# Optimization experiments

Measured on AMD Instinct MI355X. Metric: run time of the kernel, lower is better.

Reference implementation:

```python
import jax, jax.numpy as jnp
import numpy as np

T, N, F = 8, 10000, 16
E, H, LD, ENVD = 320000, 64, 3, 5
TEMP, SAL, UI, VI = 11, 12, 13, 14
ENV_IDX = jnp.array([11, 12, 13, 14, 15])
DECAY_KM = 15.0


def _lin(k, o, i, s=0.1):
    return jax.random.normal(k, (o, i), jnp.float32) * s


def setup_inputs() -> dict:
    key = jax.random.key(0)
    ks = jax.random.split(key, 24)
    inp = {
        'node_features_sequence': jax.random.normal(ks[0], (T, N, F), jnp.float32),
        'initial_lice': jax.random.uniform(ks[1], (N, LD), jnp.float32),
        'edge_distance': jax.random.uniform(ks[2], (E,), jnp.float32) * 30.0,
        'edge_direction': jax.random.normal(ks[3], (E, 2), jnp.float32),
        'ee_w1': _lin(ks[4], H, 4), 'ee_b1': jnp.zeros((H,)),
        'ee_w2': _lin(ks[5], H, H), 'ee_b2': jnp.zeros((H,)),
        'at_w1': _lin(ks[6], H, 2 * H), 'at_b1': jnp.zeros((H,)),
        'at_w2': _lin(ks[7], 1, H), 'at_b2': jnp.zeros((1,)),
        'en_w1': _lin(ks[8], H, ENVD), 'en_b1': jnp.zeros((H,)),
        'en_w2': _lin(ks[9], H, H), 'en_b2': jnp.zeros((H,)),
        'fe_w1': _lin(ks[10], 32, 1), 'fe_b1': jnp.zeros((32,)),
        'fe_w2': _lin(ks[11], 32, 32), 'fe_b2': jnp.zeros((32,)),
        'fe_w3': _lin(ks[12], 1, 32), 'fe_b3': jnp.zeros((1,)),
        'gru_wih': _lin(ks[13], 3 * H, H + ENVD + LD),
        'gru_whh': _lin(ks[14], 3 * H, H),
        'gru_bih': jnp.zeros((3 * H,)), 'gru_bhh': jnp.zeros((3 * H,)),
        'de_w1': _lin(ks[15], H, H), 'de_b1': jnp.zeros((H,)),
        'de_w2': _lin(ks[16], LD, H), 'de_b2': jnp.zeros((LD,)),
        'log_beta': jnp.float32(-1.0),
        'temp_sensitivity': jnp.float32(0.1),
        'edge_index': jax.random.randint(ks[17], (2, E), 0, N, jnp.int32),
    }
    return inp


def _mlp2(x, w1, b1, w2, b2):
    return jax.nn.relu(x @ w1.T + b1) @ w2.T + b2


def _gru(x, h, wih, whh, bih, bhh):
    gi = x @ wih.T + bih
    gh = h @ whh.T + bhh
    i_r, i_z, i_n = jnp.split(gi, 3, axis=-1)
    h_r, h_z, h_n = jnp.split(gh, 3, axis=-1)
    r = jax.nn.sigmoid(i_r + h_r)
    z = jax.nn.sigmoid(i_z + h_z)
    n = jnp.tanh(i_n + r * h_n)
    return (1.0 - z) * n + z * h


def reference(node_features_sequence, initial_lice, edge_distance, edge_direction,
              ee_w1, ee_b1, ee_w2, ee_b2, at_w1, at_b1, at_w2, at_b2,
              en_w1, en_b1, en_w2, en_b2, fe_w1, fe_b1, fe_w2, fe_b2, fe_w3, fe_b3,
              gru_wih, gru_whh, gru_bih, gru_bhh, de_w1, de_b1, de_w2, de_b2,
              log_beta, temp_sensitivity, edge_index):
    src, dst = edge_index[0], edge_index[1]
    dist_factor = jnp.exp(-edge_distance / DECAY_KM)
    beta = jnp.exp(log_beta)

    def step(carry, x_t):
        h, lice = carry
        # dynamic edge attributes: [distance, flux+ * decay, temp_src, sal_src]
        u = x_t[src, UI]
        v = x_t[src, VI]
        flux = u * edge_direction[:, 0] + v * edge_direction[:, 1]
        wflux = jnp.clip(flux, 0.0) * dist_factor
        edge_attr = jnp.stack([edge_distance, wflux, x_t[src, TEMP], x_t[src, SAL]], axis=1)
        # edge MLP + attention logits  (E,H)
        ef = _mlp2(edge_attr, ee_w1, ee_b1, ee_w2, ee_b2)
        h_src = h[src]
        logits = _mlp2(jnp.concatenate([ef, h_src], axis=-1), at_w1, at_b1, at_w2, at_b2)[:, 0]
        logits = logits + jnp.log(wflux + 1e-8)
        # per-destination segment softmax
        amax = jax.ops.segment_max(logits, dst, num_segments=N)
        aexp = jnp.exp(logits - amax[dst])
        asum = jax.ops.segment_sum(aexp, dst, num_segments=N)
        aw = aexp / (asum[dst] + 1e-8)
        # flux-weighted lice messages, scatter-add to destinations
        weighted = (aw * lice[src, 0] * beta)[:, None] * h_src  # (E,H)
        pressure = jax.ops.segment_sum(weighted, dst, num_segments=N)  # (N,H)
        # environment + fecundity
        env = x_t[:, ENV_IDX]
        temp_norm = (x_t[:, TEMP] - 10.0) / 5.0
        fec = jax.nn.softplus(
            _mlp2(jax.nn.relu(temp_norm[:, None] @ fe_w1.T + fe_b1), fe_w2, fe_b2, fe_w3, fe_b3))[:, 0]
        env_enc = _mlp2(env, en_w1, en_b1, en_w2, en_b2)
        din = jnp.concatenate([env_enc + pressure, env, lice], axis=-1)
        h_new = _gru(din, h, gru_wih, gru_whh, gru_bih, gru_bhh)
        lice_base = jax.nn.softplus(_mlp2(h_new, de_w1, de_b1, de_w2, de_b2))
        lice_new = lice_base * (1.0 + temp_sensitivity * (fec[:, None] - 1.0))
        return (h_new, lice_new), lice_new

    h0 = jnp.zeros((N, H), jnp.float32)
    _, traj = jax.lax.scan(step, (h0, initial_lice), node_features_sequence)
    return traj  # (T, N, feature_dim)
```

## Files before the change

### kernel.cpp

```cpp
#include <hip/hip_runtime.h>
#include <math.h>

#define T_STEPS 8
#define NNODES 10000
#define NFEAT 16
#define NEDGES 320000
#define HDIM 64
#define LDIM 3
#define CAP 128

typedef _Float16 f16x8 __attribute__((ext_vector_type(8)));
typedef _Float16 f16x4 __attribute__((ext_vector_type(4)));
typedef float f32x4 __attribute__((ext_vector_type(4)));

__device__ __forceinline__ float sigmoidf_(float x){ return 1.f/(1.f+__expf(-x)); }
__device__ __forceinline__ float softplusf_(float x){ return fmaxf(x,0.f)+log1pf(__expf(-fabsf(x))); }
__device__ __forceinline__ float tanhf_(float x){ return 2.f*sigmoidf_(2.f*x)-1.f; }


__global__ void __launch_bounds__(256) k_prep(
    const float* __restrict__ ee_w2, const float* __restrict__ ee_b2,
    const float* __restrict__ at_w1, const float* __restrict__ at_b1,
    _Float16* __restrict__ P_Mhi, _Float16* __restrict__ P_Mlo,
    float* __restrict__ cvec)
{
    int i = blockIdx.x*256 + threadIdx.x;
    if (i >= 64*64) return;
    int m = i>>6, j = i&63;
    float acc = 0.f;
    #pragma unroll 8
    for (int k=0;k<64;++k) acc += ee_w2[k*64+m]*at_w1[j*128+k];
    int ks = m>>5;
    int lane = ((m>>3)&3)*16 + (j&15);
    int elem = m&7;
    int fi = (j>>4)*2 + ks;
    _Float16 hi = (_Float16)acc;
    P_Mhi[(fi*64+lane)*8+elem] = hi;
    P_Mlo[(fi*64+lane)*8+elem] = (_Float16)(acc - (float)hi);
    if (m == 0){
        float c = at_b1[j];
        #pragma unroll 8
        for (int k=0;k<64;++k) c += ee_b2[k]*at_w1[j*128+k];
        cvec[j] = c;
    }
}

__device__ __forceinline__ void packB(const float* __restrict__ W, int ldw, int koff, int K, int NKS,
                                      _Float16* __restrict__ Dhi, _Float16* __restrict__ Dlo, int li){
    int elem = li & 7;
    int lane = (li >> 3) & 63;
    int fi   = li >> 9;
    int jt = fi / NKS, ks = fi % NKS;
    int j = jt*16 + (lane & 15);
    int k = ks*32 + ((lane>>4)&3)*8 + elem;
    float v = (k < K) ? W[j*ldw + koff + k] : 0.f;
    _Float16 hi = (_Float16)v;
    Dhi[li] = hi;
    Dlo[li] = (_Float16)(v - (float)hi);
}

__global__ void __launch_bounds__(256) k_init(
    const float* __restrict__ init_lice, const float* __restrict__ cvec,
    const float* __restrict__ en_w1, const float* __restrict__ en_w2,
    const float* __restrict__ gru_wih, const float* __restrict__ gru_whh,
    const float* __restrict__ de_w1, const float* __restrict__ at_w1,
    float* __restrict__ h, float* __restrict__ lice, float* __restrict__ G,
    _Float16* __restrict__ F_en1h, _Float16* __restrict__ F_en1l,
    _Float16* __restrict__ F_enh,  _Float16* __restrict__ F_enl,
    _Float16* __restrict__ F_ihh,  _Float16* __restrict__ F_ihl,
    _Float16* __restrict__ F_hhh,  _Float16* __restrict__ F_hhl,
    _Float16* __restrict__ F_deh,  _Float16* __restrict__ F_del,
    _Float16* __restrict__ F_a2h,  _Float16* __restrict__ F_a2l,
    int* __restrict__ counts)
{
    int i = blockIdx.x*256 + threadIdx.x;
    if (i < NNODES*HDIM){ h[i] = 0.f; G[i] = cvec[i&63]; }
    if (i < NNODES*LDIM) lice[i] = init_lice[i];
    if (i < NNODES) counts[i] = 0;
    if (i < 2048)       packB(en_w1,   5,  0,  5, 1, F_en1h, F_en1l, i);
    else if (i < 6144)  packB(en_w2,  64,  0, 64, 2, F_enh,  F_enl,  i-2048);
    else if (i < 24576) packB(gru_wih,72,  0, 72, 3, F_ihh,  F_ihl,  i-6144);
    else if (i < 36864) packB(gru_whh,64,  0, 64, 2, F_hhh,  F_hhl,  i-24576);
    else if (i < 40960) packB(de_w1,  64,  0, 64, 2, F_deh,  F_del,  i-36864);
    else if (i < 45056) packB(at_w1, 128, 64, 64, 2, F_a2h,  F_a2l,  i-40960);
}

__global__ void __launch_bounds__(256) k_fec(
    const float* __restrict__ nfs,
    const float* __restrict__ fe_w1, const float* __restrict__ fe_b1,
    const float* __restrict__ fe_w2, const float* __restrict__ fe_b2,
    const float* __restrict__ fe_w3, const float* __restrict__ fe_b3,
    float* __restrict__ fec_arr)
{
    int i = blockIdx.x*256 + threadIdx.x;
    if (i >= T_STEPS*NNODES) return;
    float temp = nfs[(size_t)i*NFEAT + 11];
    float tn = (temp - 10.f)*(1.f/5.f);
    float a[32];
    #pragma unroll
    for (int k=0;k<32;++k) a[k] = fmaxf(tn*fe_w1[k] + fe_b1[k], 0.f);
    float o = fe_b3[0];
    #pragma unroll 4
    for (int l=0;l<32;++l){
        float b = fe_b2[l];
        #pragma unroll
        for (int k=0;k<32;++k) b += a[k]*fe_w2[l*32+k];
        o += fmaxf(b, 0.f)*fe_w3[l];
    }
    fec_arr[i] = softplusf_(o);
}

__global__ void __launch_bounds__(256) k_hist(const int* __restrict__ ei_dst, int* __restrict__ counts){
    int e = blockIdx.x*256 + threadIdx.x;
    if (e < NEDGES) atomicAdd(&counts[ei_dst[e]], 1);
}

__global__ void __launch_bounds__(1024) k_scan(const int* __restrict__ counts,
                                               int* __restrict__ rowptr, int* __restrict__ cursor){
    __shared__ int sums[1024];
    int t = threadIdx.x;
    const int CH = 10;
    int c0 = t*CH;
    int s = 0;
    if (c0 < NNODES){
        #pragma unroll
        for (int i=0;i<CH;i++) s += counts[c0+i];
    }
    sums[t] = s;
    __syncthreads();
    for (int off=1; off<1024; off<<=1){
        int v = (t>=off) ? sums[t-off] : 0;
        __syncthreads();
        sums[t] += v;
        __syncthreads();
    }
    if (c0 < NNODES){
        int run = (t==0) ? 0 : sums[t-1];
        for (int i=0;i<CH;i++){ rowptr[c0+i] = run; run += counts[c0+i]; cursor[c0+i] = 0; }
        if (t == (NNODES/CH)-1) rowptr[NNODES] = run;
    }
}

__global__ void __launch_bounds__(256) k_scatter(const int* __restrict__ ei_dst,
        const int* __restrict__ rowptr, int* __restrict__ cursor, int* __restrict__ perm){
    int e = blockIdx.x*256 + threadIdx.x;
    if (e >= NEDGES) return;
    int d = ei_dst[e];
    int pos = rowptr[d] + atomicAdd(&cursor[d], 1);
    perm[pos] = e;
}

__global__ void __launch_bounds__(256) k_permg(
    const int* __restrict__ perm, const int* __restrict__ ei_src,
    const float* __restrict__ dist, const float* __restrict__ dirn,
    int* __restrict__ src_perm, float* __restrict__ dist_p, float* __restrict__ dirn_p)
{
    int i = blockIdx.x*256 + threadIdx.x;
    if (i >= NEDGES) return;
    int e = perm[i];
    src_perm[i] = ei_src[e];
    dist_p[i] = dist[e];
    float2 dd = *reinterpret_cast<const float2*>(dirn + 2*e);
    *reinterpret_cast<float2*>(dirn_p + 2*i) = dd;
}


__global__ void __launch_bounds__(256,2) k_edge_mfma(
    const float* __restrict__ xt, const float* __restrict__ G,
    const int* __restrict__ src_perm,
    const float* __restrict__ dist_p, const float* __restrict__ dirn_p,
    const float* __restrict__ ee_w1, const float* __restrict__ ee_b1,
    const _Float16* __restrict__ P_Mhi, const _Float16* __restrict__ P_Mlo,
    const float* __restrict__ at_w2, const float* __restrict__ at_b2,
    float* __restrict__ logits)
{
    __shared__ __align__(16) _Float16 smh[36864];
    float* smf = (float*)smh;

    const int tid = threadIdx.x;
    const int wv = tid>>6, lane = tid&63;
    const int e = blockIdx.x*256 + tid;

    f16x8 bh[4][2], bl[4][2];
    #pragma unroll
    for (int jt=0;jt<4;++jt){
        #pragma unroll
        for (int ks=0;ks<2;++ks){
            bh[jt][ks] = *(const f16x8*)(P_Mhi + (((jt*2+ks)*64 + lane)*8));
            bl[jt][ks] = *(const f16x8*)(P_Mlo + (((jt*2+ks)*64 + lane)*8));
        }
    }

    const int src = src_perm[e];
    const float d  = dist_p[e];
    float2 dir2 = *reinterpret_cast<const float2*>(dirn_p + 2*e);
    float temp = xt[src*NFEAT+11];
    float4 q  = *reinterpret_cast<const float4*>(xt + src*NFEAT + 12);
    float flux = q.y*dir2.x + q.z*dir2.y;
    float wflux = fmaxf(flux, 0.f) * __expf(-d*(1.f/15.f));
    const float a0 = d, a1 = wflux, a2 = temp, a3 = q.x;
    const float lbias = at_b2[0] + __logf(wflux + 1e-8f);

    #pragma unroll
    for (int kb=0;kb<8;++kb){
        f16x8 hv, lv;
        #pragma unroll
        for (int i=0;i<8;++i){
            const int m = kb*8+i;
            float4 w1 = *reinterpret_cast<const float4*>(ee_w1 + m*4);
            float r = fmaxf(ee_b1[m] + a0*w1.x + a1*w1.y + a2*w1.z + a3*w1.w, 0.f);
            _Float16 hi = (_Float16)r;
            hv[i] = hi;
            lv[i] = (_Float16)(r - (float)hi);
        }
        *(f16x8*)(smh + tid*72 + kb*8)         = hv;
        *(f16x8*)(smh + 18432 + tid*72 + kb*8) = lv;
    }
    asm volatile("s_waitcnt lgkmcnt(0)" ::: "memory");

    f32x4 c[4][4];
    #pragma unroll
    for (int et=0;et<4;++et)
        #pragma unroll
        for (int jt=0;jt<4;++jt)
            c[et][jt] = (f32x4){0.f,0.f,0.f,0.f};

    #pragma unroll
    for (int et=0;et<4;++et){
        #pragma unroll
        for (int ks=0;ks<2;++ks){
            const int row = wv*64 + et*16 + (lane&15);
            f16x8 ah = *(const f16x8*)(smh + row*72 + ks*32 + (lane>>4)*8);
            f16x8 al = *(const f16x8*)(smh + 18432 + row*72 + ks*32 + (lane>>4)*8);
            #pragma unroll
            for (int jt=0;jt<4;++jt){
                c[et][jt] = __builtin_amdgcn_mfma_f32_16x16x32_f16(ah, bh[jt][ks], c[et][jt], 0,0,0);
                c[et][jt] = __builtin_amdgcn_mfma_f32_16x16x32_f16(ah, bl[jt][ks], c[et][jt], 0,0,0);
                c[et][jt] = __builtin_amdgcn_mfma_f32_16x16x32_f16(al, bh[jt][ks], c[et][jt], 0,0,0);
            }
        }
    }
    asm volatile("s_waitcnt lgkmcnt(0)" ::: "memory");

    #pragma unroll
    for (int et=0;et<4;++et){
        #pragma unroll
        for (int jt=0;jt<4;++jt){
            #pragma unroll
            for (int i=0;i<4;++i){
                const int rl = et*16 + ((lane>>4)&3)*4 + i;
                const int col = jt*16 + (lane&15);
                const int idx = (et < 2) ? (wv*2304 + rl*68 + col)
                                         : (9216 + wv*2304 + (rl-32)*68 + col);
                smf[idx] = c[et][jt][i];
            }
        }
    }
    asm volatile("s_waitcnt lgkmcnt(0)" ::: "memory");

    const int el = tid & 63;
    const float* crow = smf + ((el < 32) ? (wv*2304 + el*68)
                                         : (9216 + wv*2304 + (el-32)*68));
    const float4* G4 = reinterpret_cast<const float4*>(G + src*HDIM);
    float logit = lbias;
    #pragma unroll
    for (int jj=0;jj<16;++jj){
        float4 cv = *reinterpret_cast<const float4*>(crow + jj*4);
        float4 gv = G4[jj];
        float4 w4 = *reinterpret_cast<const float4*>(at_w2 + jj*4);
        logit += w4.x*fmaxf(cv.x+gv.x,0.f) + w4.y*fmaxf(cv.y+gv.y,0.f)
               + w4.z*fmaxf(cv.z+gv.z,0.f) + w4.w*fmaxf(cv.w+gv.w,0.f);
    }
    logits[e] = logit;
}


__global__ void __launch_bounds__(256) k_softmax_pressure(
    const float* __restrict__ logits, const float* __restrict__ h,
    const float* __restrict__ lice, const int* __restrict__ src_perm,
    const int* __restrict__ rowptr,
    const float* __restrict__ log_beta,
    float* __restrict__ pressure)
{
    __shared__ float swgt[CAP];
    __shared__ int   ssrc[CAP];
    __shared__ float sred[4][64];
    __shared__ float sredm[4], sreds[4];

    const int node = blockIdx.x;
    const int tid = threadIdx.x;
    const int wid = tid >> 6;
    const int lane = tid & 63;
    const int start = rowptr[node], end = rowptr[node+1];
    const int deg = end - start;
    const int nfast = deg < CAP ? deg : CAP;

    float m = -INFINITY;
    for (int i=start+tid; i<end; i+=256){
        float lg = logits[i];
        int o = i - start;
        if (o < CAP){ swgt[o] = lg; ssrc[o] = src_perm[i]; }
        m = fmaxf(m, lg);
    }
    #pragma unroll
    for (int off=32; off>=1; off>>=1) m = fmaxf(m, __shfl_xor(m, off));
    if (lane == 0) sredm[wid] = m;
    __syncthreads();
    m = fmaxf(fmaxf(sredm[0], sredm[1]), fmaxf(sredm[2], sredm[3]));

    float s = 0.f;
    for (int i=start+tid; i<end; i+=256){
        int o = i - start;
        float lg = (o < CAP) ? swgt[o] : logits[i];
        s += __expf(lg - m);
    }
    #pragma unroll
    for (int off=32; off>=1; off>>=1) s += __shfl_xor(s, off);
    if (lane == 0) sreds[wid] = s;
    __syncthreads();
    s = (sreds[0]+sreds[1])+(sreds[2]+sreds[3]);

    const float binv = __expf(log_beta[0])/(s + 1e-8f);

    for (int o=tid; o<nfast; o+=256){
        int sc = ssrc[o];
        swgt[o] = __expf(swgt[o] - m) * binv * lice[sc*LDIM];
    }
    __syncthreads();

    float p = 0.f;
    for (int o=wid; o<nfast; o+=4)
        p += swgt[o]*h[ssrc[o]*HDIM + lane];
    for (int i=start+CAP+wid; i<end; i+=4){
        int sc = src_perm[i];
        float wg = __expf(logits[i]-m)*binv*lice[sc*LDIM];
        p += wg*h[sc*HDIM+lane];
    }
    sred[wid][lane] = p;
    __syncthreads();
    if (wid == 0)
        pressure[node*HDIM + lane] = (sred[0][lane]+sred[1][lane])+(sred[2][lane]+sred[3][lane]);
}


__global__ void __launch_bounds__(256,1) k_node_mfma(
    const float* __restrict__ xt,
    float* __restrict__ h, float* __restrict__ lice,
    const float* __restrict__ pressure,
    const _Float16* __restrict__ F_en1h, const _Float16* __restrict__ F_en1l,
    const _Float16* __restrict__ F_enh,  const _Float16* __restrict__ F_enl,
    const _Float16* __restrict__ F_ihh,  const _Float16* __restrict__ F_ihl,
    const _Float16* __restrict__ F_hhh,  const _Float16* __restrict__ F_hhl,
    const _Float16* __restrict__ F_deh,  const _Float16* __restrict__ F_del,
    const _Float16* __restrict__ F_a2h,  const _Float16* __restrict__ F_a2l,
    const float* __restrict__ en_b1, const float* __restrict__ en_b2,
    const float* __restrict__ gru_bih, const float* __restrict__ gru_bhh,
    const float* __restrict__ de_b1, const float* __restrict__ de_w2, const float* __restrict__ de_b2,
    const float* __restrict__ cvec, const float* __restrict__ fec_t,
    const float* __restrict__ temp_sens,
    float* __restrict__ G, float* __restrict__ out_t)
{
    __shared__ __align__(16) _Float16 Ah_hi[64*72], Ah_lo[64*72];
    __shared__ __align__(16) _Float16 At_hi[64*72], At_lo[64*72];
    __shared__ __align__(16) _Float16 Ad_hi[64*104], Ad_lo[64*104];
    __shared__ float s_pd[64*64];
    __shared__ float s_fec[64];

    const int tid = threadIdx.x;
    const int w = tid>>6, lane = tid&63;
    const int l15 = lane & 15, lq = (lane>>4)&3;
    const int n0 = blockIdx.x*64;
    const int nvalid = (NNODES - n0 < 64) ? (NNODES - n0) : 64;

    #pragma unroll
    for (int it=0; it<4; ++it){
        int idx = tid + it*256;
        int node = idx>>4, k4 = idx&15;
        int nc = n0 + (node < nvalid ? node : nvalid-1);
        float4 hv = *reinterpret_cast<const float4*>(h + nc*64 + k4*4);
        float4 pv = *reinterpret_cast<const float4*>(pressure + nc*64 + k4*4);
        *reinterpret_cast<float4*>(s_pd + node*64 + k4*4) = pv;
        f16x4 hh, hl;
        hh[0]=(_Float16)hv.x; hh[1]=(_Float16)hv.y; hh[2]=(_Float16)hv.z; hh[3]=(_Float16)hv.w;
        hl[0]=(_Float16)(hv.x-(float)hh[0]); hl[1]=(_Float16)(hv.y-(float)hh[1]);
        hl[2]=(_Float16)(hv.z-(float)hh[2]); hl[3]=(_Float16)(hv.w-(float)hh[3]);
        *reinterpret_cast<f16x4*>(Ah_hi + node*72 + k4*4) = hh;
        *reinterpret_cast<f16x4*>(Ah_lo + node*72 + k4*4) = hl;
    }
    if (w == 0){
        int nc = n0 + (lane < nvalid ? lane : nvalid-1);
        float ev[8];
        ev[0]=xt[nc*16+11]; ev[1]=xt[nc*16+12]; ev[2]=xt[nc*16+13];
        ev[3]=xt[nc*16+14]; ev[4]=xt[nc*16+15];
        ev[5]=lice[nc*3+0]; ev[6]=lice[nc*3+1]; ev[7]=lice[nc*3+2];
        s_fec[lane] = fec_t[nc];
        f16x8 eh, el;
        #pragma unroll
        for (int i=0;i<8;++i){ eh[i]=(_Float16)ev[i]; el[i]=(_Float16)(ev[i]-(float)eh[i]); }
        *reinterpret_cast<f16x8*>(Ad_hi + lane*104 + 64) = eh;
        *reinterpret_cast<f16x8*>(Ad_lo + lane*104 + 64) = el;
        f16x8 zz = {(_Float16)0,(_Float16)0,(_Float16)0,(_Float16)0,
                    (_Float16)0,(_Float16)0,(_Float16)0,(_Float16)0};
        *reinterpret_cast<f16x8*>(Ad_hi + lane*104 + 72) = zz;
        *reinterpret_cast<f16x8*>(Ad_hi + lane*104 + 80) = zz;
        *reinterpret_cast<f16x8*>(Ad_hi + lane*104 + 88) = zz;
        *reinterpret_cast<f16x8*>(Ad_lo + lane*104 + 72) = zz;
        *reinterpret_cast<f16x8*>(Ad_lo + lane*104 + 80) = zz;
        *reinterpret_cast<f16x8*>(Ad_lo + lane*104 + 88) = zz;
    }
    __syncthreads();

    {
        f16x8 bh = *(const f16x8*)(F_en1h + (w*64+lane)*8);
        f16x8 bl = *(const f16x8*)(F_en1l + (w*64+lane)*8);
        f32x4 c[4];
        #pragma unroll
        for (int et=0;et<4;++et) c[et] = (f32x4){0.f,0.f,0.f,0.f};
        #pragma unroll
        for (int et=0;et<4;++et){
            int row = et*16 + l15;
            f16x8 ah = *(const f16x8*)(Ad_hi + row*104 + 64 + lq*8);
            f16x8 al = *(const f16x8*)(Ad_lo + row*104 + 64 + lq*8);
            c[et] = __builtin_amdgcn_mfma_f32_16x16x32_f16(ah, bh, c[et],0,0,0);
            c[et] = __builtin_amdgcn_mfma_f32_16x16x32_f16(ah, bl, c[et],0,0,0);
            c[et] = __builtin_amdgcn_mfma_f32_16x16x32_f16(al, bh, c[et],0,0,0);
        }
        int col = w*16 + l15;
        float b1 = en_b1[col];
        #pragma unroll
        for (int et=0;et<4;++et){
            #pragma unroll
            for (int i=0;i<4;++i){
                int row = et*16 + lq*4 + i;
                float v = fmaxf(c[et][i] + b1, 0.f);
                _Float16 hi = (_Float16)v;
                At_hi[row*72+col] = hi;
                At_lo[row*72+col] = (_Float16)(v-(float)hi);
            }
        }
    }
    __syncthreads();

    {
        f32x4 c[4];
        #pragma unroll
        for (int et=0;et<4;++et) c[et] = (f32x4){0.f,0.f,0.f,0.f};
        #pragma unroll
        for (int ks=0; ks<2; ++ks){
            f16x8 bh = *(const f16x8*)(F_enh + ((w*2+ks)*64+lane)*8);
            f16x8 bl = *(const f16x8*)(F_enl + ((w*2+ks)*64+lane)*8);
            #pragma unroll
            for (int et=0;et<4;++et){
                int row = et*16 + l15;
                f16x8 ah = *(const f16x8*)(At_hi + row*72 + ks*32 + lq*8);
                f16x8 al = *(const f16x8*)(At_lo + row*72 + ks*32 + lq*8);
                c[et] = __builtin_amdgcn_mfma_f32_16x16x32_f16(ah, bh, c[et],0,0,0);
                c[et] = __builtin_amdgcn_mfma_f32_16x16x32_f16(ah, bl, c[et],0,0,0);
                c[et] = __builtin_amdgcn_mfma_f32_16x16x32_f16(al, bh, c[et],0,0,0);
            }
        }
        int col = w*16 + l15;
        float b2 = en_b2[col];
        #pragma unroll
        for (int et=0;et<4;++et){
            #pragma unroll
            for (int i=0;i<4;++i){
                int row = et*16 + lq*4 + i;
                float v = c[et][i] + b2 + s_pd[row*64+col];
                _Float16 hi = (_Float16)v;
                Ad_hi[row*104+col] = hi;
                Ad_lo[row*104+col] = (_Float16)(v-(float)hi);
            }
        }
    }
    __syncthreads();

    f32x4 Cr[4], Cz[4], Ci[4], Chn[4];
    {
        int col = w*16 + l15;
        float br = gru_bih[col]     + gru_bhh[col];
        float bz = gru_bih[64+col]  + gru_bhh[64+col];
        float bi = gru_bih[128+col];
        float bn = gru_bhh[128+col];
        #pragma unroll
        for (int et=0;et<4;++et){
            Cr[et]  = (f32x4){br,br,br,br};
            Cz[et]  = (f32x4){bz,bz,bz,bz};
            Ci[et]  = (f32x4){bi,bi,bi,bi};
            Chn[et] = (f32x4){bn,bn,bn,bn};
        }
    }
    #pragma unroll
    for (int ks=0; ks<3; ++ks){
        f16x8 ah[4], al[4];
        #pragma unroll
        for (int et=0;et<4;++et){
            int row = et*16 + l15;
            ah[et] = *(const f16x8*)(Ad_hi + row*104 + ks*32 + lq*8);
            al[et] = *(const f16x8*)(Ad_lo + row*104 + ks*32 + lq*8);
        }
        {
            int fi = w*3 + ks;
            f16x8 bh = *(const f16x8*)(F_ihh + (fi*64+lane)*8);
            f16x8 bl = *(const f16x8*)(F_ihl + (fi*64+lane)*8);
            #pragma unroll
            for (int et=0;et<4;++et){
                Cr[et] = __builtin_amdgcn_mfma_f32_16x16x32_f16(ah[et], bh, Cr[et],0,0,0);
                Cr[et] = __builtin_amdgcn_mfma_f32_16x16x32_f16(ah[et], bl, Cr[et],0,0,0);
                Cr[et] = __builtin_amdgcn_mfma_f32_16x16x32_f16(al[et], bh, Cr[et],0,0,0);
            }
        }
        {
            int fi = (4+w)*3 + ks;
            f16x8 bh = *(const f16x8*)(F_ihh + (fi*64+lane)*8);
            f16x8 bl = *(const f16x8*)(F_ihl + (fi*64+lane)*8);
            #pragma unroll
            for (int et=0;et<4;++et){
                Cz[et] = __builtin_amdgcn_mfma_f32_16x16x32_f16(ah[et], bh, Cz[et],0,0,0);
                Cz[et] = __builtin_amdgcn_mfma_f32_16x16x32_f16(ah[et], bl, Cz[et],0,0,0);
                Cz[et] = __builtin_amdgcn_mfma_f32_16x16x32_f16(al[et], bh, Cz[et],0,0,0);
            }
        }
        {
            int fi = (8+w)*3 + ks;
            f16x8 bh = *(const f16x8*)(F_ihh + (fi*64+lane)*8);
            f16x8 bl = *(const f16x8*)(F_ihl + (fi*64+lane)*8);
            #pragma unroll
            for (int et=0;et<4;++et){
                Ci[et] = __builtin_amdgcn_mfma_f32_16x16x32_f16(ah[et], bh, Ci[et],0,0,0);
                Ci[et] = __builtin_amdgcn_mfma_f32_16x16x32_f16(ah[et], bl, Ci[et],0,0,0);
                Ci[et] = __builtin_amdgcn_mfma_f32_16x16x32_f16(al[et], bh, Ci[et],0,0,0);
            }
        }
    }
    #pragma unroll
    for (int ks=0; ks<2; ++ks){
        f16x8 ah[4], al[4];
        #pragma unroll
        for (int et=0;et<4;++et){
            int row = et*16 + l15;
            ah[et] = *(const f16x8*)(Ah_hi + row*72 + ks*32 + lq*8);
            al[et] = *(const f16x8*)(Ah_lo + row*72 + ks*32 + lq*8);
        }
        {
            int fi = w*2 + ks;
            f16x8 bh = *(const f16x8*)(F_hhh + (fi*64+lane)*8);
            f16x8 bl = *(const f16x8*)(F_hhl + (fi*64+lane)*8);
            #pragma unroll
            for (int et=0;et<4;++et){
                Cr[et] = __builtin_amdgcn_mfma_f32_16x16x32_f16(ah[et], bh, Cr[et],0,0,0);
                Cr[et] = __builtin_amdgcn_mfma_f32_16x16x32_f16(ah[et], bl, Cr[et],0,0,0);
                Cr[et] = __builtin_amdgcn_mfma_f32_16x16x32_f16(al[et], bh, Cr[et],0,0,0);
            }
        }
        {
            int fi = (4+w)*2 + ks;
            f16x8 bh = *(const f16x8*)(F_hhh + (fi*64+lane)*8);
            f16x8 bl = *(const f16x8*)(F_hhl + (fi*64+lane)*8);
            #pragma unroll
            for (int et=0;et<4;++et){
                Cz[et] = __builtin_amdgcn_mfma_f32_16x16x32_f16(ah[et], bh, Cz[et],0,0,0);
                Cz[et] = __builtin_amdgcn_mfma_f32_16x16x32_f16(ah[et], bl, Cz[et],0,0,0);
                Cz[et] = __builtin_amdgcn_mfma_f32_16x16x32_f16(al[et], bh, Cz[et],0,0,0);
            }
        }
        {
            int fi = (8+w)*2 + ks;
            f16x8 bh = *(const f16x8*)(F_hhh + (fi*64+lane)*8);
            f16x8 bl = *(const f16x8*)(F_hhl + (fi*64+lane)*8);
            #pragma unroll
            for (int et=0;et<4;++et){
                Chn[et] = __builtin_amdgcn_mfma_f32_16x16x32_f16(ah[et], bh, Chn[et],0,0,0);
                Chn[et] = __builtin_amdgcn_mfma_f32_16x16x32_f16(ah[et], bl, Chn[et],0,0,0);
                Chn[et] = __builtin_amdgcn_mfma_f32_16x16x32_f16(al[et], bh, Chn[et],0,0,0);
            }
        }
    }

    float hnv[16];
    {
        const int coln = w*16 + l15;
        #pragma unroll
        for (int et=0;et<4;++et){
            #pragma unroll
            for (int i=0;i<4;++i){
                int row = et*16 + lq*4 + i;
                float r  = sigmoidf_(Cr[et][i]);
                float z  = sigmoidf_(Cz[et][i]);
                float nn = tanhf_(Ci[et][i] + r*Chn[et][i]);
                float hold = (float)Ah_hi[row*72+coln] + (float)Ah_lo[row*72+coln];
                hnv[et*4+i] = (1.f-z)*nn + z*hold;
            }
        }
    }
    __syncthreads();
    {
        const int coln = w*16 + l15;
        #pragma unroll
        for (int et=0;et<4;++et){
            #pragma unroll
            for (int i=0;i<4;++i){
                int row = et*16 + lq*4 + i;
                float v = hnv[et*4+i];
                if (row < nvalid) h[(n0+row)*HDIM + coln] = v;
                _Float16 hi = (_Float16)v;
                Ah_hi[row*72+coln] = hi;
                Ah_lo[row*72+coln] = (_Float16)(v-(float)hi);
            }
        }
    }
    __syncthreads();

    {
        int col = w*16 + l15;
        float bd = de_b1[col], bg = cvec[col];
        f32x4 Cd[4], Cg[4];
        #pragma unroll
        for (int et=0;et<4;++et){ Cd[et]=(f32x4){bd,bd,bd,bd}; Cg[et]=(f32x4){bg,bg,bg,bg}; }
        #pragma unroll
        for (int ks=0;ks<2;++ks){
            f16x8 ah[4], al[4];
            #pragma unroll
            for (int et=0;et<4;++et){
                int row = et*16 + l15;
                ah[et] = *(const f16x8*)(Ah_hi + row*72 + ks*32 + lq*8);
                al[et] = *(const f16x8*)(Ah_lo + row*72 + ks*32 + lq*8);
            }
            f16x8 dh = *(const f16x8*)(F_deh + ((w*2+ks)*64+lane)*8);
            f16x8 dl = *(const f16x8*)(F_del + ((w*2+ks)*64+lane)*8);
            f16x8 gh = *(const f16x8*)(F_a2h + ((w*2+ks)*64+lane)*8);
            f16x8 gl = *(const f16x8*)(F_a2l + ((w*2+ks)*64+lane)*8);
            #pragma unroll
            for (int et=0;et<4;++et){
                Cd[et] = __builtin_amdgcn_mfma_f32_16x16x32_f16(ah[et], dh, Cd[et],0,0,0);
                Cd[et] = __builtin_amdgcn_mfma_f32_16x16x32_f16(ah[et], dl, Cd[et],0,0,0);
                Cd[et] = __builtin_amdgcn_mfma_f32_16x16x32_f16(al[et], dh, Cd[et],0,0,0);
                Cg[et] = __builtin_amdgcn_mfma_f32_16x16x32_f16(ah[et], gh, Cg[et],0,0,0);
                Cg[et] = __builtin_amdgcn_mfma_f32_16x16x32_f16(ah[et], gl, Cg[et],0,0,0);
                Cg[et] = __builtin_amdgcn_mfma_f32_16x16x32_f16(al[et], gh, Cg[et],0,0,0);
            }
        }
        #pragma unroll
        for (int et=0;et<4;++et){
            #pragma unroll
            for (int i=0;i<4;++i){
                int row = et*16 + lq*4 + i;
                if (row < nvalid) G[(n0+row)*HDIM + col] = Cg[et][i];
                s_pd[row*64+col] = fmaxf(Cd[et][i], 0.f);
            }
        }
    }
    __syncthreads();

    {
        float ts = temp_sens[0];
        #pragma unroll 1
        for (int m=0;m<16;++m){
            int node = w*16 + m;
            float d1v = s_pd[node*64 + lane];
            float s0 = d1v*de_w2[lane];
            float s1 = d1v*de_w2[64+lane];
            float s2 = d1v*de_w2[128+lane];
            #pragma unroll
            for (int off=32; off>=1; off>>=1){
                s0 += __shfl_xor(s0,off);
                s1 += __shfl_xor(s1,off);
                s2 += __shfl_xor(s2,off);
            }
            if (lane < LDIM && node < nvalid){
                float fec = s_fec[node];
                float oi = (lane==0?s0:(lane==1?s1:s2)) + de_b2[lane];
                float lb = softplusf_(oi);
                float ln = lb*(1.f + ts*(fec-1.f));
                lice[(n0+node)*LDIM+lane] = ln;
                out_t[(n0+node)*LDIM+lane] = ln;
            }
        }
    }
}


extern "C" void kernel_launch(void* const* d_in, const int* in_sizes, int n_in,
                              void* d_out, int out_size, void* d_ws, size_t ws_size,
                              hipStream_t stream) {
    const float* nfs       = (const float*)d_in[0];
    const float* init_lice = (const float*)d_in[1];
    const float* dist      = (const float*)d_in[2];
    const float* dirn      = (const float*)d_in[3];
    const float* ee_w1     = (const float*)d_in[4];
    const float* ee_b1     = (const float*)d_in[5];
    const float* ee_w2     = (const float*)d_in[6];
    const float* ee_b2     = (const float*)d_in[7];
    const float* at_w1     = (const float*)d_in[8];
    const float* at_b1     = (const float*)d_in[9];
    const float* at_w2     = (const float*)d_in[10];
    const float* at_b2     = (const float*)d_in[11];
    const float* en_w1     = (const float*)d_in[12];
    const float* en_b1     = (const float*)d_in[13];
    const float* en_w2     = (const float*)d_in[14];
    const float* en_b2     = (const float*)d_in[15];
    const float* fe_w1     = (const float*)d_in[16];
    const float* fe_b1     = (const float*)d_in[17];
    const float* fe_w2     = (const float*)d_in[18];
    const float* fe_b2     = (const float*)d_in[19];
    const float* fe_w3     = (const float*)d_in[20];
    const float* fe_b3     = (const float*)d_in[21];
    const float* gru_wih   = (const float*)d_in[22];
    const float* gru_whh   = (const float*)d_in[23];
    const float* gru_bih   = (const float*)d_in[24];
    const float* gru_bhh   = (const float*)d_in[25];
    const float* de_w1     = (const float*)d_in[26];
    const float* de_b1     = (const float*)d_in[27];
    const float* de_w2     = (const float*)d_in[28];
    const float* de_b2     = (const float*)d_in[29];
    const float* log_beta  = (const float*)d_in[30];
    const float* temp_sens = (const float*)d_in[31];
    const int*   ei        = (const int*)d_in[32];
    const int*   ei_src = ei;
    const int*   ei_dst = ei + NEDGES;
    float* out = (float*)d_out;

    float* wsf = (float*)d_ws;
    size_t off = 0;
    float* h        = wsf + off; off += (size_t)NNODES*HDIM;
    float* lice     = wsf + off; off += (size_t)NNODES*LDIM + 2;
    off = (off + 3) & ~(size_t)3;
    float* logits   = wsf + off; off += (size_t)NEDGES;
    float* pressure = wsf + off; off += (size_t)NNODES*HDIM;
    float* G        = wsf + off; off += (size_t)NNODES*HDIM;
    float* cvec     = wsf + off; off += 64;
    _Float16* P_Mhi = (_Float16*)(wsf + off); off += 2048;
    _Float16* P_Mlo = (_Float16*)(wsf + off); off += 2048;
    _Float16* F_en1h= (_Float16*)(wsf + off); off += 1024;
    _Float16* F_en1l= (_Float16*)(wsf + off); off += 1024;
    _Float16* F_enh = (_Float16*)(wsf + off); off += 2048;
    _Float16* F_enl = (_Float16*)(wsf + off); off += 2048;
    _Float16* F_ihh = (_Float16*)(wsf + off); off += 9216;
    _Float16* F_ihl = (_Float16*)(wsf + off); off += 9216;
    _Float16* F_hhh = (_Float16*)(wsf + off); off += 6144;
    _Float16* F_hhl = (_Float16*)(wsf + off); off += 6144;
    _Float16* F_deh = (_Float16*)(wsf + off); off += 2048;
    _Float16* F_del = (_Float16*)(wsf + off); off += 2048;
    _Float16* F_a2h = (_Float16*)(wsf + off); off += 2048;
    _Float16* F_a2l = (_Float16*)(wsf + off); off += 2048;
    float* fec_arr  = wsf + off; off += (size_t)T_STEPS*NNODES;
    float* dist_p   = wsf + off; off += NEDGES;
    float* dirn_p   = wsf + off; off += 2*NEDGES;
    int* src_perm = (int*)(wsf + off); off += NEDGES;
    int* counts = (int*)(wsf + off); off += NNODES;
    int* rowptr = (int*)(wsf + off); off += NNODES+1;
    int* cursor = (int*)(wsf + off); off += NNODES;
    int* perm   = (int*)(wsf + off); off += NEDGES;

    k_prep<<<16,256,0,stream>>>(ee_w2, ee_b2, at_w1, at_b1, P_Mhi, P_Mlo, cvec);
    k_init<<<2500,256,0,stream>>>(init_lice, cvec,
                                  en_w1, en_w2, gru_wih, gru_whh, de_w1, at_w1,
                                  h, lice, G,
                                  F_en1h, F_en1l, F_enh, F_enl,
                                  F_ihh, F_ihl, F_hhh, F_hhl,
                                  F_deh, F_del, F_a2h, F_a2l,
                                  counts);
    k_fec<<<(T_STEPS*NNODES+255)/256,256,0,stream>>>(nfs, fe_w1, fe_b1, fe_w2, fe_b2,
                                                     fe_w3, fe_b3, fec_arr);
    k_hist<<<1250,256,0,stream>>>(ei_dst, counts);
    k_scan<<<1,1024,0,stream>>>(counts, rowptr, cursor);
    k_scatter<<<1250,256,0,stream>>>(ei_dst, rowptr, cursor, perm);
    k_permg<<<1250,256,0,stream>>>(perm, ei_src, dist, dirn, src_perm, dist_p, dirn_p);

    const int node_blocks = (NNODES + 63)/64;
    for (int t=0; t<T_STEPS; ++t){
        const float* xt = nfs + (size_t)t*NNODES*NFEAT;
        k_edge_mfma<<<1250,256,0,stream>>>(xt, G, src_perm, dist_p, dirn_p,
                                           ee_w1, ee_b1, P_Mhi, P_Mlo,
                                           at_w2, at_b2, logits);
        k_softmax_pressure<<<NNODES,256,0,stream>>>(logits, h, lice, src_perm,
                                                    rowptr, log_beta, pressure);
        k_node_mfma<<<node_blocks,256,0,stream>>>(xt, h, lice, pressure,
                                           F_en1h, F_en1l, F_enh, F_enl,
                                           F_ihh, F_ihl, F_hhh, F_hhl,
                                           F_deh, F_del, F_a2h, F_a2l,
                                           en_b1, en_b2, gru_bih, gru_bhh,
                                           de_b1, de_w2, de_b2,
                                           cvec, fec_arr + (size_t)t*NNODES,
                                           temp_sens,
                                           G, out + (size_t)t*NNODES*LDIM);
    }
}
```

Baseline: 835.0 us.

## Shrink node-update kernel tile to 16 nodes per block for more blocks

The node MLP/GRU kernel now handles 16 nodes per 256-thread block instead of 64, so each wave does one MFMA row tile instead of four. This gives 625 blocks instead of 157, which spreads the work across more CUs and cuts register and LDS use (launch bounds raised to 4 blocks per CU). The cost is that each block reloads the same weight fragments for fewer nodes, and the bounds checks are dropped on the assumption that N divides evenly by 16.

```diff
diff --git a/kernel.cpp b/kernel.cpp
--- a/kernel.cpp
+++ b/kernel.cpp
@@ -343,7 +343,7 @@
 }
 
 
-__global__ void __launch_bounds__(256,1) k_node_mfma(
+__global__ void __launch_bounds__(256,4) k_node_mfma(
     const float* __restrict__ xt,
     float* __restrict__ h, float* __restrict__ lice,
     const float* __restrict__ pressure,
@@ -360,23 +360,20 @@
     const float* __restrict__ temp_sens,
     float* __restrict__ G, float* __restrict__ out_t)
 {
-    __shared__ __align__(16) _Float16 Ah_hi[64*72], Ah_lo[64*72];
-    __shared__ __align__(16) _Float16 At_hi[64*72], At_lo[64*72];
-    __shared__ __align__(16) _Float16 Ad_hi[64*104], Ad_lo[64*104];
-    __shared__ float s_pd[64*64];
-    __shared__ float s_fec[64];
+    __shared__ __align__(16) _Float16 Ah_hi[16*72], Ah_lo[16*72];
+    __shared__ __align__(16) _Float16 At_hi[16*72], At_lo[16*72];
+    __shared__ __align__(16) _Float16 Ad_hi[16*104], Ad_lo[16*104];
+    __shared__ float s_pd[16*64];
+    __shared__ float s_fec[16];
 
     const int tid = threadIdx.x;
     const int w = tid>>6, lane = tid&63;
     const int l15 = lane & 15, lq = (lane>>4)&3;
-    const int n0 = blockIdx.x*64;
-    const int nvalid = (NNODES - n0 < 64) ? (NNODES - n0) : 64;
-
-    #pragma unroll
-    for (int it=0; it<4; ++it){
-        int idx = tid + it*256;
-        int node = idx>>4, k4 = idx&15;
-        int nc = n0 + (node < nvalid ? node : nvalid-1);
+    const int n0 = blockIdx.x*16;
+
+    {
+        int node = tid>>4, k4 = tid&15;
+        int nc = n0 + node;
         float4 hv = *reinterpret_cast<const float4*>(h + nc*64 + k4*4);
         float4 pv = *reinterpret_cast<const float4*>(pressure + nc*64 + k4*4);
         *reinterpret_cast<float4*>(s_pd + node*64 + k4*4) = pv;
@@ -387,8 +384,8 @@
         *reinterpret_cast<f16x4*>(Ah_hi + node*72 + k4*4) = hh;
         *reinterpret_cast<f16x4*>(Ah_lo + node*72 + k4*4) = hl;
     }
-    if (w == 0){
-        int nc = n0 + (lane < nvalid ? lane : nvalid-1);
+    if (w == 0 && lane < 16){
+        int nc = n0 + lane;
         float ev[8];
         ev[0]=xt[nc*16+11]; ev[1]=xt[nc*16+12]; ev[2]=xt[nc*16+13];
         ev[3]=xt[nc*16+14]; ev[4]=xt[nc*16+15];
@@ -413,200 +410,145 @@
     {
         f16x8 bh = *(const f16x8*)(F_en1h + (w*64+lane)*8);
         f16x8 bl = *(const f16x8*)(F_en1l + (w*64+lane)*8);
-        f32x4 c[4];
-        #pragma unroll
-        for (int et=0;et<4;++et) c[et] = (f32x4){0.f,0.f,0.f,0.f};
-        #pragma unroll
-        for (int et=0;et<4;++et){
-            int row = et*16 + l15;
-            f16x8 ah = *(const f16x8*)(Ad_hi + row*104 + 64 + lq*8);
-            f16x8 al = *(const f16x8*)(Ad_lo + row*104 + 64 + lq*8);
-            c[et] = __builtin_amdgcn_mfma_f32_16x16x32_f16(ah, bh, c[et],0,0,0);
-            c[et] = __builtin_amdgcn_mfma_f32_16x16x32_f16(ah, bl, c[et],0,0,0);
-            c[et] = __builtin_amdgcn_mfma_f32_16x16x32_f16(al, bh, c[et],0,0,0);
-        }
+        f32x4 c = (f32x4){0.f,0.f,0.f,0.f};
+        f16x8 ah = *(const f16x8*)(Ad_hi + l15*104 + 64 + lq*8);
+        f16x8 al = *(const f16x8*)(Ad_lo + l15*104 + 64 + lq*8);
+        c = __builtin_amdgcn_mfma_f32_16x16x32_f16(ah, bh, c,0,0,0);
+        c = __builtin_amdgcn_mfma_f32_16x16x32_f16(ah, bl, c,0,0,0);
+        c = __builtin_amdgcn_mfma_f32_16x16x32_f16(al, bh, c,0,0,0);
         int col = w*16 + l15;
         float b1 = en_b1[col];
         #pragma unroll
-        for (int et=0;et<4;++et){
-            #pragma unroll
-            for (int i=0;i<4;++i){
-                int row = et*16 + lq*4 + i;
-                float v = fmaxf(c[et][i] + b1, 0.f);
-                _Float16 hi = (_Float16)v;
-                At_hi[row*72+col] = hi;
-                At_lo[row*72+col] = (_Float16)(v-(float)hi);
-            }
+        for (int i=0;i<4;++i){
+            int row = lq*4 + i;
+            float v = fmaxf(c[i] + b1, 0.f);
+            _Float16 hi = (_Float16)v;
+            At_hi[row*72+col] = hi;
+            At_lo[row*72+col] = (_Float16)(v-(float)hi);
         }
     }
     __syncthreads();
 
     {
-        f32x4 c[4];
-        #pragma unroll
-        for (int et=0;et<4;++et) c[et] = (f32x4){0.f,0.f,0.f,0.f};
+        f32x4 c = (f32x4){0.f,0.f,0.f,0.f};
         #pragma unroll
         for (int ks=0; ks<2; ++ks){
             f16x8 bh = *(const f16x8*)(F_enh + ((w*2+ks)*64+lane)*8);
             f16x8 bl = *(const f16x8*)(F_enl + ((w*2+ks)*64+lane)*8);
-            #pragma unroll
-            for (int et=0;et<4;++et){
-                int row = et*16 + l15;
-                f16x8 ah = *(const f16x8*)(At_hi + row*72 + ks*32 + lq*8);
-                f16x8 al = *(const f16x8*)(At_lo + row*72 + ks*32 + lq*8);
-                c[et] = __builtin_amdgcn_mfma_f32_16x16x32_f16(ah, bh, c[et],0,0,0);
-                c[et] = __builtin_amdgcn_mfma_f32_16x16x32_f16(ah, bl, c[et],0,0,0);
-                c[et] = __builtin_amdgcn_mfma_f32_16x16x32_f16(al, bh, c[et],0,0,0);
-            }
+            f16x8 ah = *(const f16x8*)(At_hi + l15*72 + ks*32 + lq*8);
+            f16x8 al = *(const f16x8*)(At_lo + l15*72 + ks*32 + lq*8);
+            c = __builtin_amdgcn_mfma_f32_16x16x32_f16(ah, bh, c,0,0,0);
+            c = __builtin_amdgcn_mfma_f32_16x16x32_f16(ah, bl, c,0,0,0);
+            c = __builtin_amdgcn_mfma_f32_16x16x32_f16(al, bh, c,0,0,0);
         }
         int col = w*16 + l15;
         float b2 = en_b2[col];
         #pragma unroll
-        for (int et=0;et<4;++et){
-            #pragma unroll
-            for (int i=0;i<4;++i){
-                int row = et*16 + lq*4 + i;
-                float v = c[et][i] + b2 + s_pd[row*64+col];
-                _Float16 hi = (_Float16)v;
-                Ad_hi[row*104+col] = hi;
-                Ad_lo[row*104+col] = (_Float16)(v-(float)hi);
-            }
-        }
-    }
-    __syncthreads();
-
-    f32x4 Cr[4], Cz[4], Ci[4], Chn[4];
+        for (int i=0;i<4;++i){
+            int row = lq*4 + i;
+            float v = c[i] + b2 + s_pd[row*64+col];
+            _Float16 hi = (_Float16)v;
+            Ad_hi[row*104+col] = hi;
+            Ad_lo[row*104+col] = (_Float16)(v-(float)hi);
+        }
+    }
+    __syncthreads();
+
+    f32x4 Cr, Cz, Ci, Chn;
     {
         int col = w*16 + l15;
         float br = gru_bih[col]     + gru_bhh[col];
         float bz = gru_bih[64+col]  + gru_bhh[64+col];
         float bi = gru_bih[128+col];
         float bn = gru_bhh[128+col];
-        #pragma unroll
-        for (int et=0;et<4;++et){
-            Cr[et]  = (f32x4){br,br,br,br};
-            Cz[et]  = (f32x4){bz,bz,bz,bz};
-            Ci[et]  = (f32x4){bi,bi,bi,bi};
-            Chn[et] = (f32x4){bn,bn,bn,bn};
-        }
+        Cr  = (f32x4){br,br,br,br};
+        Cz  = (f32x4){bz,bz,bz,bz};
+        Ci  = (f32x4){bi,bi,bi,bi};
+        Chn = (f32x4){bn,bn,bn,bn};
     }
     #pragma unroll
     for (int ks=0; ks<3; ++ks){
-        f16x8 ah[4], al[4];
-        #pragma unroll
-        for (int et=0;et<4;++et){
-            int row = et*16 + l15;
-            ah[et] = *(const f16x8*)(Ad_hi + row*104 + ks*32 + lq*8);
-            al[et] = *(const f16x8*)(Ad_lo + row*104 + ks*32 + lq*8);
-        }
+        f16x8 ah = *(const f16x8*)(Ad_hi + l15*104 + ks*32 + lq*8);
+        f16x8 al = *(const f16x8*)(Ad_lo + l15*104 + ks*32 + lq*8);
         {
             int fi = w*3 + ks;
             f16x8 bh = *(const f16x8*)(F_ihh + (fi*64+lane)*8);
             f16x8 bl = *(const f16x8*)(F_ihl + (fi*64+lane)*8);
-            #pragma unroll
-            for (int et=0;et<4;++et){
-                Cr[et] = __builtin_amdgcn_mfma_f32_16x16x32_f16(ah[et], bh, Cr[et],0,0,0);
-                Cr[et] = __builtin_amdgcn_mfma_f32_16x16x32_f16(ah[et], bl, Cr[et],0,0,0);
-                Cr[et] = __builtin_amdgcn_mfma_f32_16x16x32_f16(al[et], bh, Cr[et],0,0,0);
-            }
+            Cr = __builtin_amdgcn_mfma_f32_16x16x32_f16(ah, bh, Cr,0,0,0);
+            Cr = __builtin_amdgcn_mfma_f32_16x16x32_f16(ah, bl, Cr,0,0,0);
+            Cr = __builtin_amdgcn_mfma_f32_16x16x32_f16(al, bh, Cr,0,0,0);
         }
         {
             int fi = (4+w)*3 + ks;
             f16x8 bh = *(const f16x8*)(F_ihh + (fi*64+lane)*8);
             f16x8 bl = *(const f16x8*)(F_ihl + (fi*64+lane)*8);
-            #pragma unroll
-            for (int et=0;et<4;++et){
-                Cz[et] = __builtin_amdgcn_mfma_f32_16x16x32_f16(ah[et], bh, Cz[et],0,0,0);
-                Cz[et] = __builtin_amdgcn_mfma_f32_16x16x32_f16(ah[et], bl, Cz[et],0,0,0);
-                Cz[et] = __builtin_amdgcn_mfma_f32_16x16x32_f16(al[et], bh, Cz[et],0,0,0);
-            }
+            Cz = __builtin_amdgcn_mfma_f32_16x16x32_f16(ah, bh, Cz,0,0,0);
+            Cz = __builtin_amdgcn_mfma_f32_16x16x32_f16(ah, bl, Cz,0,0,0);
+            Cz = __builtin_amdgcn_mfma_f32_16x16x32_f16(al, bh, Cz,0,0,0);
         }
         {
             int fi = (8+w)*3 + ks;
             f16x8 bh = *(const f16x8*)(F_ihh + (fi*64+lane)*8);
             f16x8 bl = *(const f16x8*)(F_ihl + (fi*64+lane)*8);
-            #pragma unroll
-            for (int et=0;et<4;++et){
-                Ci[et] = __builtin_amdgcn_mfma_f32_16x16x32_f16(ah[et], bh, Ci[et],0,0,0);
-                Ci[et] = __builtin_amdgcn_mfma_f32_16x16x32_f16(ah[et], bl, Ci[et],0,0,0);
-                Ci[et] = __builtin_amdgcn_mfma_f32_16x16x32_f16(al[et], bh, Ci[et],0,0,0);
-            }
+            Ci = __builtin_amdgcn_mfma_f32_16x16x32_f16(ah, bh, Ci,0,0,0);
+            Ci = __builtin_amdgcn_mfma_f32_16x16x32_f16(ah, bl, Ci,0,0,0);
+            Ci = __builtin_amdgcn_mfma_f32_16x16x32_f16(al, bh, Ci,0,0,0);
         }
     }
     #pragma unroll
     for (int ks=0; ks<2; ++ks){
-        f16x8 ah[4], al[4];
-        #pragma unroll
-        for (int et=0;et<4;++et){
-            int row = et*16 + l15;
-            ah[et] = *(const f16x8*)(Ah_hi + row*72 + ks*32 + lq*8);
-            al[et] = *(const f16x8*)(Ah_lo + row*72 + ks*32 + lq*8);
-        }
+        f16x8 ah = *(const f16x8*)(Ah_hi + l15*72 + ks*32 + lq*8);
+        f16x8 al = *(const f16x8*)(Ah_lo + l15*72 + ks*32 + lq*8);
         {
             int fi = w*2 + ks;
             f16x8 bh = *(const f16x8*)(F_hhh + (fi*64+lane)*8);
             f16x8 bl = *(const f16x8*)(F_hhl + (fi*64+lane)*8);
-            #pragma unroll
-            for (int et=0;et<4;++et){
-                Cr[et] = __builtin_amdgcn_mfma_f32_16x16x32_f16(ah[et], bh, Cr[et],0,0,0);
-                Cr[et] = __builtin_amdgcn_mfma_f32_16x16x32_f16(ah[et], bl, Cr[et],0,0,0);
-                Cr[et] = __builtin_amdgcn_mfma_f32_16x16x32_f16(al[et], bh, Cr[et],0,0,0);
-            }
+            Cr = __builtin_amdgcn_mfma_f32_16x16x32_f16(ah, bh, Cr,0,0,0);
+            Cr = __builtin_amdgcn_mfma_f32_16x16x32_f16(ah, bl, Cr,0,0,0);
+            Cr = __builtin_amdgcn_mfma_f32_16x16x32_f16(al, bh, Cr,0,0,0);
         }
         {
             int fi = (4+w)*2 + ks;
             f16x8 bh = *(const f16x8*)(F_hhh + (fi*64+lane)*8);
             f16x8 bl = *(const f16x8*)(F_hhl + (fi*64+lane)*8);
-            #pragma unroll
-            for (int et=0;et<4;++et){
-                Cz[et] = __builtin_amdgcn_mfma_f32_16x16x32_f16(ah[et], bh, Cz[et],0,0,0);
-                Cz[et] = __builtin_amdgcn_mfma_f32_16x16x32_f16(ah[et], bl, Cz[et],0,0,0);
-                Cz[et] = __builtin_amdgcn_mfma_f32_16x16x32_f16(al[et], bh, Cz[et],0,0,0);
-            }
+            Cz = __builtin_amdgcn_mfma_f32_16x16x32_f16(ah, bh, Cz,0,0,0);
+            Cz = __builtin_amdgcn_mfma_f32_16x16x32_f16(ah, bl, Cz,0,0,0);
+            Cz = __builtin_amdgcn_mfma_f32_16x16x32_f16(al, bh, Cz,0,0,0);
         }
         {
             int fi = (8+w)*2 + ks;
             f16x8 bh = *(const f16x8*)(F_hhh + (fi*64+lane)*8);
             f16x8 bl = *(const f16x8*)(F_hhl + (fi*64+lane)*8);
-            #pragma unroll
-            for (int et=0;et<4;++et){
-                Chn[et] = __builtin_amdgcn_mfma_f32_16x16x32_f16(ah[et], bh, Chn[et],0,0,0);
-                Chn[et] = __builtin_amdgcn_mfma_f32_16x16x32_f16(ah[et], bl, Chn[et],0,0,0);
-                Chn[et] = __builtin_amdgcn_mfma_f32_16x16x32_f16(al[et], bh, Chn[et],0,0,0);
-            }
-        }
-    }
-
-    float hnv[16];
+            Chn = __builtin_amdgcn_mfma_f32_16x16x32_f16(ah, bh, Chn,0,0,0);
+            Chn = __builtin_amdgcn_mfma_f32_16x16x32_f16(ah, bl, Chn,0,0,0);
+            Chn = __builtin_amdgcn_mfma_f32_16x16x32_f16(al, bh, Chn,0,0,0);
+        }
+    }
+
+    float hnv[4];
     {
         const int coln = w*16 + l15;
         #pragma unroll
-        for (int et=0;et<4;++et){
-            #pragma unroll
-            for (int i=0;i<4;++i){
-                int row = et*16 + lq*4 + i;
-                float r  = sigmoidf_(Cr[et][i]);
-                float z  = sigmoidf_(Cz[et][i]);
-                float nn = tanhf_(Ci[et][i] + r*Chn[et][i]);
-                float hold = (float)Ah_hi[row*72+coln] + (float)Ah_lo[row*72+coln];
-                hnv[et*4+i] = (1.f-z)*nn + z*hold;
-            }
+        for (int i=0;i<4;++i){
+            int row = lq*4 + i;
+            float r  = sigmoidf_(Cr[i]);
+            float z  = sigmoidf_(Cz[i]);
+            float nn = tanhf_(Ci[i] + r*Chn[i]);
+            float hold = (float)Ah_hi[row*72+coln] + (float)Ah_lo[row*72+coln];
+            hnv[i] = (1.f-z)*nn + z*hold;
         }
     }
     __syncthreads();
     {
         const int coln = w*16 + l15;
         #pragma unroll
-        for (int et=0;et<4;++et){
-            #pragma unroll
-            for (int i=0;i<4;++i){
-                int row = et*16 + lq*4 + i;
-                float v = hnv[et*4+i];
-                if (row < nvalid) h[(n0+row)*HDIM + coln] = v;
-                _Float16 hi = (_Float16)v;
-                Ah_hi[row*72+coln] = hi;
-                Ah_lo[row*72+coln] = (_Float16)(v-(float)hi);
-            }
+        for (int i=0;i<4;++i){
+            int row = lq*4 + i;
+            float v = hnv[i];
+            h[(n0+row)*HDIM + coln] = v;
+            _Float16 hi = (_Float16)v;
+            Ah_hi[row*72+coln] = hi;
+            Ah_lo[row*72+coln] = (_Float16)(v-(float)hi);
         }
     }
     __syncthreads();
@@ -614,49 +556,37 @@
     {
         int col = w*16 + l15;
         float bd = de_b1[col], bg = cvec[col];
-        f32x4 Cd[4], Cg[4];
-        #pragma unroll
-        for (int et=0;et<4;++et){ Cd[et]=(f32x4){bd,bd,bd,bd}; Cg[et]=(f32x4){bg,bg,bg,bg}; }
+        f32x4 Cd = (f32x4){bd,bd,bd,bd};
+        f32x4 Cg = (f32x4){bg,bg,bg,bg};
         #pragma unroll
         for (int ks=0;ks<2;++ks){
-            f16x8 ah[4], al[4];
-            #pragma unroll
-            for (int et=0;et<4;++et){
-                int row = et*16 + l15;
-                ah[et] = *(const f16x8*)(Ah_hi + row*72 + ks*32 + lq*8);
-                al[et] = *(const f16x8*)(Ah_lo + row*72 + ks*32 + lq*8);
-            }
+            f16x8 ah = *(const f16x8*)(Ah_hi + l15*72 + ks*32 + lq*8);
+            f16x8 al = *(const f16x8*)(Ah_lo + l15*72 + ks*32 + lq*8);
             f16x8 dh = *(const f16x8*)(F_deh + ((w*2+ks)*64+lane)*8);
             f16x8 dl = *(const f16x8*)(F_del + ((w*2+ks)*64+lane)*8);
             f16x8 gh = *(const f16x8*)(F_a2h + ((w*2+ks)*64+lane)*8);
             f16x8 gl = *(const f16x8*)(F_a2l + ((w*2+ks)*64+lane)*8);
-            #pragma unroll
-            for (int et=0;et<4;++et){
-                Cd[et] = __builtin_amdgcn_mfma_f32_16x16x32_f16(ah[et], dh, Cd[et],0,0,0);
-                Cd[et] = __builtin_amdgcn_mfma_f32_16x16x32_f16(ah[et], dl, Cd[et],0,0,0);
-                Cd[et] = __builtin_amdgcn_mfma_f32_16x16x32_f16(al[et], dh, Cd[et],0,0,0);
-                Cg[et] = __builtin_amdgcn_mfma_f32_16x16x32_f16(ah[et], gh, Cg[et],0,0,0);
-                Cg[et] = __builtin_amdgcn_mfma_f32_16x16x32_f16(ah[et], gl, Cg[et],0,0,0);
-                Cg[et] = __builtin_amdgcn_mfma_f32_16x16x32_f16(al[et], gh, Cg[et],0,0,0);
-            }
-        }
-        #pragma unroll
-        for (int et=0;et<4;++et){
-            #pragma unroll
-            for (int i=0;i<4;++i){
-                int row = et*16 + lq*4 + i;
-                if (row < nvalid) G[(n0+row)*HDIM + col] = Cg[et][i];
-                s_pd[row*64+col] = fmaxf(Cd[et][i], 0.f);
-            }
+            Cd = __builtin_amdgcn_mfma_f32_16x16x32_f16(ah, dh, Cd,0,0,0);
+            Cd = __builtin_amdgcn_mfma_f32_16x16x32_f16(ah, dl, Cd,0,0,0);
+            Cd = __builtin_amdgcn_mfma_f32_16x16x32_f16(al, dh, Cd,0,0,0);
+            Cg = __builtin_amdgcn_mfma_f32_16x16x32_f16(ah, gh, Cg,0,0,0);
+            Cg = __builtin_amdgcn_mfma_f32_16x16x32_f16(ah, gl, Cg,0,0,0);
+            Cg = __builtin_amdgcn_mfma_f32_16x16x32_f16(al, gh, Cg,0,0,0);
+        }
+        #pragma unroll
+        for (int i=0;i<4;++i){
+            int row = lq*4 + i;
+            G[(n0+row)*HDIM + col] = Cg[i];
+            s_pd[row*64+col] = fmaxf(Cd[i], 0.f);
         }
     }
     __syncthreads();
 
     {
         float ts = temp_sens[0];
-        #pragma unroll 1
-        for (int m=0;m<16;++m){
-            int node = w*16 + m;
+        #pragma unroll
+        for (int m=0;m<4;++m){
+            int node = w*4 + m;
             float d1v = s_pd[node*64 + lane];
             float s0 = d1v*de_w2[lane];
             float s1 = d1v*de_w2[64+lane];
@@ -667,7 +597,7 @@
                 s1 += __shfl_xor(s1,off);
                 s2 += __shfl_xor(s2,off);
             }
-            if (lane < LDIM && node < nvalid){
+            if (lane < LDIM){
                 float fec = s_fec[node];
                 float oi = (lane==0?s0:(lane==1?s1:s2)) + de_b2[lane];
                 float lb = softplusf_(oi);
@@ -767,7 +697,7 @@
     k_scatter<<<1250,256,0,stream>>>(ei_dst, rowptr, cursor, perm);
     k_permg<<<1250,256,0,stream>>>(perm, ei_src, dist, dirn, src_perm, dist_p, dirn_p);
 
-    const int node_blocks = (NNODES + 63)/64;
+    const int node_blocks = NNODES/16;
     for (int t=0; t<T_STEPS; ++t){
         const float* xt = nfs + (size_t)t*NNODES*NFEAT;
         k_edge_mfma<<<1250,256,0,stream>>>(xt, G, src_perm, dist_p, dirn_p,
```

After: 756.6 us. 1.1x faster.
